# Performance work log

Measured on AMD Instinct MI355X. Metric: run time of the kernel, lower is better.

Reference implementation:

```python
import jax, jax.numpy as jnp
import numpy as np

N = 50000      # nodes
E = 800000     # edges (before self loops)
FE = 256       # expression features
FC = 128       # CNV features
H = 128        # hidden_channels
NC = 8         # num_classes
C = 512        # number of central nodes


def setup_inputs() -> dict:
    key = jax.random.key(0)
    ks = jax.random.split(key, 24)

    def lin(k, fi, fo):
        k1, k2 = jax.random.split(k)
        s = 1.0 / np.sqrt(fi)
        W = jax.random.uniform(k1, (fi, fo), jnp.float32, -s, s)
        b = jax.random.uniform(k2, (fo,), jnp.float32, -s, s)
        return W, b

    x = jax.random.normal(ks[0], (N, FE), jnp.float32)
    c = jax.random.normal(ks[1], (N, FC), jnp.float32)
    edge_index = jax.random.randint(ks[2], (2, E), 0, N, jnp.int32)
    central_idx = jax.random.randint(ks[3], (C,), 0, N, jnp.int32)

    W1e, b1e = lin(ks[4], FE, H)
    W2e, b2e = lin(ks[5], H, H)
    W1c, b1c = lin(ks[6], FC, H)
    W2c, b2c = lin(ks[7], H, H)
    Wm, bm = lin(ks[8], 2 * H, NC)
    Wp1, bp1 = lin(ks[9], NC, H)
    Wp2, bp2 = lin(ks[10], H, NC)

    return dict(
        x=x, c=c, edge_index=edge_index, central_idx=central_idx,
        me_x=jax.random.normal(ks[11], (FE,), jnp.float32),
        me_c=jax.random.normal(ks[12], (FC,), jnp.float32),
        W1e=W1e, b1e=b1e, eps1e=jnp.float32(0.0),
        W2e=W2e, b2e=b2e, eps2e=jnp.float32(0.0),
        W1c=W1c, b1c=b1c, eps1c=jnp.float32(0.0),
        W2c=W2c, b2c=b2c, eps2c=jnp.float32(0.0),
        Wm=Wm, bm=bm, Wp1=Wp1, bp1=bp1, Wp2=Wp2, bp2=bp2,
    )


def _gin_conv(h, src, dst, eps, W, b):
    # GINConv with nn = Linear: lin((1+eps)*x + sum_{j in N(i)} x_j)
    agg = jax.ops.segment_sum(h[src], dst, num_segments=N)  # scatter-add of messages
    return ((1.0 + eps) * h + agg) @ W + b


def reference(x, c, edge_index, central_idx, me_x, me_c,
              W1e, b1e, eps1e, W2e, b2e, eps2e,
              W1c, b1c, eps1c, W2c, b2c, eps2c,
              Wm, bm, Wp1, bp1, Wp2, bp2):
    lrelu = lambda v: jax.nn.leaky_relu(v, 0.2)

    # add self loops
    loops = jnp.arange(N, dtype=edge_index.dtype)
    src = jnp.concatenate([edge_index[0], loops])
    dst = jnp.concatenate([edge_index[1], loops])

    # replace exact-zero entries with learned missing embeddings (broadcast per row)
    x = jnp.where(x == 0, me_x[None, :], x)
    c = jnp.where(c == 0, me_c[None, :], c)

    x_exp = lrelu(_gin_conv(x, src, dst, eps1e, W1e, b1e))
    x_exp = lrelu(_gin_conv(x_exp, src, dst, eps2e, W2e, b2e))

    x_cnv = lrelu(_gin_conv(c, src, dst, eps1c, W1c, b1c))
    x_cnv = lrelu(_gin_conv(x_cnv, src, dst, eps2c, W2c, b2c))

    h = jnp.concatenate([x_exp, x_cnv], axis=1)          # [N, 2H]
    out = lrelu(h @ Wm + bm)                             # [N, NC]

    central = out[central_idx]                           # [C, NC]
    logits = jax.nn.relu(central @ Wp1 + bp1) @ Wp2 + bp2
    return out, logits
```

## Files before the change

### kernel.cpp

```cpp
#include <hip/hip_runtime.h>

typedef unsigned short u16;
typedef __attribute__((ext_vector_type(8))) short short8;
typedef __attribute__((ext_vector_type(4))) float floatx4;

__device__ __forceinline__ float b2f(unsigned int ubits) {
  union { unsigned int i; float f; } cv; cv.i = ubits << 16; return cv.f;
}
__device__ __forceinline__ float hi2f(unsigned int u) {
  union { unsigned int i; float f; } cv; cv.i = u & 0xffff0000u; return cv.f;
}
__device__ __forceinline__ float lo2f(unsigned int u) {
  union { unsigned int i; float f; } cv; cv.i = u << 16; return cv.f;
}
__device__ __forceinline__ u16 f2b(float f) {
  unsigned int u = __builtin_bit_cast(unsigned int, f);
  u += 0x7fffu + ((u >> 16) & 1u);
  return (u16)(u >> 16);
}
__device__ __forceinline__ float lrelu(float v) { return v > 0.f ? v : 0.2f * v; }
__device__ __forceinline__ float rdf(bool isbf, const void* p, int idx) {
  return isbf ? b2f((unsigned int)((const u16*)p)[idx]) : ((const float*)p)[idx];
}

__global__ __launch_bounds__(256) void init_kernel(int* __restrict__ deg, int n,
                                                   const u16* __restrict__ probe,
                                                   int* __restrict__ flag) {
  int i0 = (blockIdx.x * 256 + threadIdx.x) * 4;
  if (i0 + 3 < n) {
    *(int4*)(deg + i0) = make_int4(0, 0, 0, 0);
  } else {
    for (int j = 0; j < 4; j++) if (i0 + j < n) deg[i0 + j] = 0;
  }
  if (blockIdx.x == 0 && threadIdx.x < 64) {
    int lane = threadIdx.x;
    int cnt = 0;
    for (int i = lane; i < 256; i += 64) {
      unsigned int u = probe[i];
      unsigned int e = (u >> 7) & 0xFFu;
      if ((u & 0x7fffu) == 0 || (e >= 60 && e <= 191)) cnt++;
    }
#pragma unroll
    for (int off = 32; off; off >>= 1) cnt += __shfl_down(cnt, off, 64);
    if (lane == 0) *flag = (cnt >= 240) ? 1 : 0;
  }
}

__global__ __launch_bounds__(256) void hist_kernel(const int* __restrict__ dst, int E,
                                                   int* __restrict__ deg) {
  int i = blockIdx.x * 256 + threadIdx.x;
  if (i < E) atomicAdd(deg + dst[i], 1);
}

#define SCB 1024

__global__ __launch_bounds__(256) void scan_phaseA(const int* __restrict__ deg,
                                                   int* __restrict__ bsum, int n) {
  int i0 = blockIdx.x * SCB + threadIdx.x * 4;
  int s = 0;
  if (i0 + 3 < n) {
    int4 v = *(const int4*)(deg + i0);
    s = v.x + v.y + v.z + v.w;
  } else {
    for (int j = 0; j < 4; j++) if (i0 + j < n) s += deg[i0 + j];
  }
#pragma unroll
  for (int off = 32; off; off >>= 1) s += __shfl_down(s, off, 64);
  __shared__ int ws4[4];
  int lane = threadIdx.x & 63, wid = threadIdx.x >> 6;
  if (lane == 0) ws4[wid] = s;
  __syncthreads();
  if (threadIdx.x == 0) bsum[blockIdx.x] = ws4[0] + ws4[1] + ws4[2] + ws4[3];
}

__global__ void scan_phaseB(const int* __restrict__ bsum, int* __restrict__ boff,
                            int PB, int* __restrict__ rowptr, int n) {
  int lane = threadIdx.x;
  int v = (lane < PB) ? bsum[lane] : 0;
  int incl = v;
#pragma unroll
  for (int off = 1; off < 64; off <<= 1) {
    int t = __shfl_up(incl, off, 64);
    if (lane >= off) incl += t;
  }
  if (lane < PB) boff[lane] = incl - v;
  if (lane == 63) rowptr[n] = incl;
}

__global__ __launch_bounds__(256) void scan_phaseC(const int* __restrict__ deg,
                                                   const int* __restrict__ boff,
                                                   int* __restrict__ rowptr,
                                                   int* __restrict__ cursor, int n) {
  int i0 = blockIdx.x * SCB + threadIdx.x * 4;
  int v0 = 0, v1 = 0, v2 = 0, v3 = 0;
  if (i0 + 3 < n) {
    int4 v = *(const int4*)(deg + i0);
    v0 = v.x; v1 = v.y; v2 = v.z; v3 = v.w;
  } else {
    if (i0 < n) v0 = deg[i0];
    if (i0 + 1 < n) v1 = deg[i0 + 1];
    if (i0 + 2 < n) v2 = deg[i0 + 2];
    if (i0 + 3 < n) v3 = deg[i0 + 3];
  }
  int local = v0 + v1 + v2 + v3;
  int lane = threadIdx.x & 63, wid = threadIdx.x >> 6;
  int incl = local;
#pragma unroll
  for (int off = 1; off < 64; off <<= 1) {
    int t = __shfl_up(incl, off, 64);
    if (lane >= off) incl += t;
  }
  __shared__ int ws4[4];
  if (lane == 63) ws4[wid] = incl;
  __syncthreads();
  int woff = 0;
  for (int w = 0; w < wid; w++) woff += ws4[w];
  int run = boff[blockIdx.x] + woff + incl - local;
  if (i0 < n)     { rowptr[i0] = run;     cursor[i0] = run; }     run += v0;
  if (i0 + 1 < n) { rowptr[i0 + 1] = run; cursor[i0 + 1] = run; } run += v1;
  if (i0 + 2 < n) { rowptr[i0 + 2] = run; cursor[i0 + 2] = run; } run += v2;
  if (i0 + 3 < n) { rowptr[i0 + 3] = run; cursor[i0 + 3] = run; }
}

__global__ __launch_bounds__(256) void fill_kernel(const int* __restrict__ src,
                                                   const int* __restrict__ dst, int E,
                                                   int* __restrict__ cursor,
                                                   int* __restrict__ colarr) {
  int i = blockIdx.x * 256 + threadIdx.x;
  if (i < E) {
    int p = atomicAdd(cursor + dst[i], 1);
    colarr[p] = src[i];
  }
}

struct TWDesc {
  const void* W[5];
  int K[5];
  int Nc[5];
  int base[6];
};

__global__ __launch_bounds__(256) void transpose_all(TWDesc d, u16* __restrict__ out,
                                                     const int* __restrict__ flagp) {
  bool isbf = (*flagp != 0);
  int idx = blockIdx.x * 256 + threadIdx.x;
  if (idx >= d.base[5]) return;
  int s = 0;
  while (idx >= d.base[s + 1]) s++;
  int local = idx - d.base[s];
  int K = d.K[s], Nc = d.Nc[s];
  int nn = local / K;
  int k = local - nn * K;
  out[idx] = (nn < Nc) ? f2b(rdf(isbf, d.W[s], k * Nc + nn)) : (u16)0;
}

__device__ __forceinline__ short8 load_a_me(const void* Av, int lda, const void* me,
                                            int r, int k0, int q, bool isbf) {
  short8 a;
  if (isbf) {
    a = *(const short8*)((const u16*)Av + (long)r * lda + k0 + q * 8);
#pragma unroll
    for (int j = 0; j < 8; j++) {
      if (((u16)a[j] & 0x7fffu) == 0)
        a[j] = (short)((const u16*)me)[k0 + q * 8 + j];
    }
  } else {
    const float* A = (const float*)Av;
    const uint4* p = (const uint4*)(A + (long)r * lda + k0 + q * 8);
    uint4 w0 = p[0];
    uint4 w1 = p[1];
    unsigned int ww[8] = {w0.x, w0.y, w0.z, w0.w, w1.x, w1.y, w1.z, w1.w};
#pragma unroll
    for (int j = 0; j < 8; j++) {
      if ((ww[j] & 0x7fffffffu) == 0)
        a[j] = (short)f2b(((const float*)me)[k0 + q * 8 + j]);
      else
        a[j] = (short)f2b(__builtin_bit_cast(float, ww[j]));
    }
  }
  return a;
}

__global__ __launch_bounds__(256) void gemm_l1(
    const void* __restrict__ x, const void* __restrict__ cc,
    const void* __restrict__ mex, const void* __restrict__ mec,
    const u16* __restrict__ w1e_t, const u16* __restrict__ w1c_t,
    int M, u16* __restrict__ tb, const int* __restrict__ flagp) {
  bool isbf = (*flagp != 0);
  int wid = threadIdx.x >> 6;
  int lane = threadIdx.x & 63;
  int l15 = lane & 15;
  int q = lane >> 4;
  int row0 = blockIdx.x * 64 + wid * 16;
  int r = row0 + l15;
  if (r >= M) r = M - 1;

  floatx4 acce[8], accc[8];
#pragma unroll
  for (int n = 0; n < 8; n++) { acce[n] = (floatx4){0,0,0,0}; accc[n] = (floatx4){0,0,0,0}; }

  for (int k0 = 0; k0 < 256; k0 += 32) {
    short8 a = load_a_me(x, 256, mex, r, k0, q, isbf);
#pragma unroll
    for (int n = 0; n < 8; n++) {
      short8 b = *(const short8*)(w1e_t + (n * 16 + l15) * 256 + k0 + q * 8);
      acce[n] = __builtin_amdgcn_mfma_f32_16x16x32_bf16(a, b, acce[n], 0, 0, 0);
    }
  }
  for (int k0 = 0; k0 < 128; k0 += 32) {
    short8 a = load_a_me(cc, 128, mec, r, k0, q, isbf);
#pragma unroll
    for (int n = 0; n < 8; n++) {
      short8 b = *(const short8*)(w1c_t + (n * 16 + l15) * 128 + k0 + q * 8);
      accc[n] = __builtin_amdgcn_mfma_f32_16x16x32_bf16(a, b, accc[n], 0, 0, 0);
    }
  }
#pragma unroll
  for (int n = 0; n < 8; n++)
#pragma unroll
    for (int rr = 0; rr < 4; rr++) {
      int row = row0 + q * 4 + rr;
      if (row < M) {
        tb[(long)row * 256 + n * 16 + l15] = f2b(acce[n][rr]);
        tb[(long)row * 256 + 128 + n * 16 + l15] = f2b(accc[n][rr]);
      }
    }
}

__global__ __launch_bounds__(256) void gemm_l2(
    const u16* __restrict__ u,
    const u16* __restrict__ w2e_t, const u16* __restrict__ w2c_t,
    int M, u16* __restrict__ tb) {
  int wid = threadIdx.x >> 6;
  int lane = threadIdx.x & 63;
  int l15 = lane & 15;
  int q = lane >> 4;
  int row0 = blockIdx.x * 64 + wid * 16;
  int r = row0 + l15;
  if (r >= M) r = M - 1;

  floatx4 acce[8], accc[8];
#pragma unroll
  for (int n = 0; n < 8; n++) { acce[n] = (floatx4){0,0,0,0}; accc[n] = (floatx4){0,0,0,0}; }

  for (int k0 = 0; k0 < 128; k0 += 32) {
    short8 ae = *(const short8*)(u + (long)r * 256 + k0 + q * 8);
    short8 ac = *(const short8*)(u + (long)r * 256 + 128 + k0 + q * 8);
#pragma unroll
    for (int n = 0; n < 8; n++) {
      short8 be = *(const short8*)(w2e_t + (n * 16 + l15) * 128 + k0 + q * 8);
      short8 bc = *(const short8*)(w2c_t + (n * 16 + l15) * 128 + k0 + q * 8);
      acce[n] = __builtin_amdgcn_mfma_f32_16x16x32_bf16(ae, be, acce[n], 0, 0, 0);
      accc[n] = __builtin_amdgcn_mfma_f32_16x16x32_bf16(ac, bc, accc[n], 0, 0, 0);
    }
  }
#pragma unroll
  for (int n = 0; n < 8; n++)
#pragma unroll
    for (int rr = 0; rr < 4; rr++) {
      int row = row0 + q * 4 + rr;
      if (row < M) {
        tb[(long)row * 256 + n * 16 + l15] = f2b(acce[n][rr]);
        tb[(long)row * 256 + 128 + n * 16 + l15] = f2b(accc[n][rr]);
      }
    }
}

__global__ __launch_bounds__(256) void agg_kernel(
    const u16* __restrict__ t, const int* __restrict__ rowptr, const int* __restrict__ colarr,
    const void* __restrict__ epsE, const void* __restrict__ epsC,
    const void* __restrict__ bE, const void* __restrict__ bC,
    u16* __restrict__ u, int N, const int* __restrict__ flagp) {
  int node = blockIdx.x * 4 + (threadIdx.x >> 6);
  if (node >= N) return;
  bool isbf = (*flagp != 0);
  int lane = threadIdx.x & 63;
  int f0 = lane << 2;
  const u16* tb = t + f0;
  float a0 = 0.f, a1 = 0.f, a2 = 0.f, a3 = 0.f;
  int e = rowptr[node], e1 = rowptr[node + 1];
  for (; e + 4 <= e1; e += 4) {
    int c0 = colarr[e], c1 = colarr[e + 1], c2 = colarr[e + 2], c3 = colarr[e + 3];
    uint2 p0 = *(const uint2*)(tb + ((long)c0 << 8));
    uint2 p1 = *(const uint2*)(tb + ((long)c1 << 8));
    uint2 p2 = *(const uint2*)(tb + ((long)c2 << 8));
    uint2 p3 = *(const uint2*)(tb + ((long)c3 << 8));
    a0 += lo2f(p0.x); a1 += hi2f(p0.x); a2 += lo2f(p0.y); a3 += hi2f(p0.y);
    a0 += lo2f(p1.x); a1 += hi2f(p1.x); a2 += lo2f(p1.y); a3 += hi2f(p1.y);
    a0 += lo2f(p2.x); a1 += hi2f(p2.x); a2 += lo2f(p2.y); a3 += hi2f(p2.y);
    a0 += lo2f(p3.x); a1 += hi2f(p3.x); a2 += lo2f(p3.y); a3 += hi2f(p3.y);
  }
  for (; e < e1; e++) {
    int c = colarr[e];
    uint2 p = *(const uint2*)(tb + ((long)c << 8));
    a0 += lo2f(p.x); a1 += hi2f(p.x); a2 += lo2f(p.y); a3 += hi2f(p.y);
  }
  uint2 ps = *(const uint2*)(tb + ((long)node << 8));
  bool isE = (lane < 32);
  float eps2 = 2.0f + rdf(isbf, isE ? epsE : epsC, 0);
  const void* bp = isE ? bE : bC;
  int bi = isE ? f0 : (f0 - 128);
  a0 = lrelu(a0 + eps2 * lo2f(ps.x) + rdf(isbf, bp, bi + 0));
  a1 = lrelu(a1 + eps2 * hi2f(ps.x) + rdf(isbf, bp, bi + 1));
  a2 = lrelu(a2 + eps2 * lo2f(ps.y) + rdf(isbf, bp, bi + 2));
  a3 = lrelu(a3 + eps2 * hi2f(ps.y) + rdf(isbf, bp, bi + 3));
  uint2 o;
  o.x = ((unsigned int)f2b(a1) << 16) | f2b(a0);
  o.y = ((unsigned int)f2b(a3) << 16) | f2b(a2);
  *(uint2*)(u + ((long)node << 8) + f0) = o;
}

__global__ __launch_bounds__(256) void agg_head(
    const u16* __restrict__ t, const int* __restrict__ rowptr, const int* __restrict__ colarr,
    const void* __restrict__ epsE, const void* __restrict__ epsC,
    const void* __restrict__ bE, const void* __restrict__ bC,
    const u16* __restrict__ wm_t, const void* __restrict__ bm,
    float* __restrict__ out, int N, const int* __restrict__ flagp) {
  __shared__ float wmf[2048];
  __shared__ float bmf[8];
  bool isbf = (*flagp != 0);
  int tid = threadIdx.x;
  for (int i = tid; i < 2048; i += 256) wmf[i] = b2f((unsigned int)wm_t[i]);
  if (tid < 8) bmf[tid] = rdf(isbf, bm, tid);
  __syncthreads();

  int node = blockIdx.x * 4 + (tid >> 6);
  if (node >= N) return;
  int lane = tid & 63;
  int f0 = lane << 2;
  const u16* tb = t + f0;
  float a0 = 0.f, a1 = 0.f, a2 = 0.f, a3 = 0.f;
  int e = rowptr[node], e1 = rowptr[node + 1];
  for (; e + 4 <= e1; e += 4) {
    int c0 = colarr[e], c1 = colarr[e + 1], c2 = colarr[e + 2], c3 = colarr[e + 3];
    uint2 p0 = *(const uint2*)(tb + ((long)c0 << 8));
    uint2 p1 = *(const uint2*)(tb + ((long)c1 << 8));
    uint2 p2 = *(const uint2*)(tb + ((long)c2 << 8));
    uint2 p3 = *(const uint2*)(tb + ((long)c3 << 8));
    a0 += lo2f(p0.x); a1 += hi2f(p0.x); a2 += lo2f(p0.y); a3 += hi2f(p0.y);
    a0 += lo2f(p1.x); a1 += hi2f(p1.x); a2 += lo2f(p1.y); a3 += hi2f(p1.y);
    a0 += lo2f(p2.x); a1 += hi2f(p2.x); a2 += lo2f(p2.y); a3 += hi2f(p2.y);
    a0 += lo2f(p3.x); a1 += hi2f(p3.x); a2 += lo2f(p3.y); a3 += hi2f(p3.y);
  }
  for (; e < e1; e++) {
    int c = colarr[e];
    uint2 p = *(const uint2*)(tb + ((long)c << 8));
    a0 += lo2f(p.x); a1 += hi2f(p.x); a2 += lo2f(p.y); a3 += hi2f(p.y);
  }
  uint2 ps = *(const uint2*)(tb + ((long)node << 8));
  bool isE = (lane < 32);
  float eps2 = 2.0f + rdf(isbf, isE ? epsE : epsC, 0);
  const void* bp = isE ? bE : bC;
  int bi = isE ? f0 : (f0 - 128);
  a0 = lrelu(a0 + eps2 * lo2f(ps.x) + rdf(isbf, bp, bi + 0));
  a1 = lrelu(a1 + eps2 * hi2f(ps.x) + rdf(isbf, bp, bi + 1));
  a2 = lrelu(a2 + eps2 * lo2f(ps.y) + rdf(isbf, bp, bi + 2));
  a3 = lrelu(a3 + eps2 * hi2f(ps.y) + rdf(isbf, bp, bi + 3));

  float p[8];
#pragma unroll
  for (int col = 0; col < 8; col++) {
    float4 w = *(const float4*)&wmf[col * 256 + f0];
    p[col] = a0 * w.x + a1 * w.y + a2 * w.z + a3 * w.w;
  }
#pragma unroll
  for (int m = 1; m < 64; m <<= 1) {
#pragma unroll
    for (int col = 0; col < 8; col++) p[col] += __shfl_xor(p[col], m, 64);
  }
  if (lane == 0) {
    float4 o0, o1;
    o0.x = lrelu(p[0] + bmf[0]); o0.y = lrelu(p[1] + bmf[1]);
    o0.z = lrelu(p[2] + bmf[2]); o0.w = lrelu(p[3] + bmf[3]);
    o1.x = lrelu(p[4] + bmf[4]); o1.y = lrelu(p[5] + bmf[5]);
    o1.z = lrelu(p[6] + bmf[6]); o1.w = lrelu(p[7] + bmf[7]);
    *(float4*)(out + (long)node * 8) = o0;
    *(float4*)(out + (long)node * 8 + 4) = o1;
  }
}

__global__ __launch_bounds__(128) void mlp_kernel(
    const float* __restrict__ outbuf, const int* __restrict__ central,
    const void* __restrict__ Wp1, const void* __restrict__ bp1,
    const void* __restrict__ Wp2, const void* __restrict__ bp2,
    float* __restrict__ logits, const int* __restrict__ flagp) {
  __shared__ float h1[128];
  __shared__ float o[8];
  bool isbf = (*flagp != 0);
  int b = blockIdx.x, tid = threadIdx.x;
  int node = central[b];
  if (tid < 8) o[tid] = outbuf[node * 8 + tid];
  __syncthreads();
  float s = rdf(isbf, bp1, tid);
#pragma unroll
  for (int k = 0; k < 8; k++) s += o[k] * rdf(isbf, Wp1, k * 128 + tid);
  h1[tid] = fmaxf(s, 0.f);
  __syncthreads();
  if (tid < 8) {
    float s2 = rdf(isbf, bp2, tid);
    for (int k = 0; k < 128; k++) s2 += h1[k] * rdf(isbf, Wp2, k * 8 + tid);
    logits[b * 8 + tid] = s2;
  }
}

extern "C" void kernel_launch(void* const* d_in, const int* in_sizes, int n_in,
                              void* d_out, int out_size, void* d_ws, size_t ws_size,
                              hipStream_t stream) {
  const void* x    = d_in[0];
  const void* c    = d_in[1];
  const int* eidx  = (const int*)d_in[2];
  const int* cidx  = (const int*)d_in[3];
  const void* me_x = d_in[4];
  const void* me_c = d_in[5];
  const void* W1e  = d_in[6];
  const void* b1e  = d_in[7];
  const void* e1e  = d_in[8];
  const void* W2e  = d_in[9];
  const void* b2e  = d_in[10];
  const void* e2e  = d_in[11];
  const void* W1c  = d_in[12];
  const void* b1c  = d_in[13];
  const void* e1c  = d_in[14];
  const void* W2c  = d_in[15];
  const void* b2c  = d_in[16];
  const void* e2c  = d_in[17];
  const void* Wm   = d_in[18];
  const void* bm   = d_in[19];
  const void* Wp1  = d_in[20];
  const void* bp1  = d_in[21];
  const void* Wp2  = d_in[22];
  const void* bp2  = d_in[23];

  const int N = in_sizes[0] / 256;
  const int E = in_sizes[2] / 2;
  const int Cn = in_sizes[3];
  const int* src = eidx;
  const int* dst = eidx + E;

  char* ws = (char*)d_ws;
  int* deg    = (int*)(ws + 0);
  int* rowptr = (int*)(ws + 200192);
  int* cursor = (int*)(ws + 400384);
  int* colarr = (int*)(ws + 600576);
  u16* tbuf   = (u16*)(ws + 3800576);
  u16* ubuf   = (u16*)(ws + 29400576);
  u16* wt_all = (u16*)(ws + 55000576);
  int* flag   = (int*)(ws + 55172608);
  int* bsum   = (int*)(ws + 55172864);
  int* boff   = (int*)(ws + 55173120);

  u16* w1e_t = wt_all + 0;
  u16* w1c_t = wt_all + 32768;
  u16* w2e_t = wt_all + 49152;
  u16* w2c_t = wt_all + 65536;
  u16* wm_t  = wt_all + 81920;

  init_kernel<<<(N + 1023) / 1024, 256, 0, stream>>>(deg, N, (const u16*)x, flag);

  hist_kernel<<<(E + 255) / 256, 256, 0, stream>>>(dst, E, deg);
  int PB = (N + SCB - 1) / SCB;
  scan_phaseA<<<PB, 256, 0, stream>>>(deg, bsum, N);
  scan_phaseB<<<1, 64, 0, stream>>>(bsum, boff, PB, rowptr, N);
  scan_phaseC<<<PB, 256, 0, stream>>>(deg, boff, rowptr, cursor, N);
  fill_kernel<<<(E + 255) / 256, 256, 0, stream>>>(src, dst, E, cursor, colarr);

  TWDesc td;
  td.W[0] = W1e; td.K[0] = 256; td.Nc[0] = 128;
  td.W[1] = W1c; td.K[1] = 128; td.Nc[1] = 128;
  td.W[2] = W2e; td.K[2] = 128; td.Nc[2] = 128;
  td.W[3] = W2c; td.K[3] = 128; td.Nc[3] = 128;
  td.W[4] = Wm;  td.K[4] = 256; td.Nc[4] = 8;
  td.base[0] = 0; td.base[1] = 32768; td.base[2] = 49152;
  td.base[3] = 65536; td.base[4] = 81920; td.base[5] = 86016;
  transpose_all<<<(86016 + 255) / 256, 256, 0, stream>>>(td, wt_all, flag);

  int gb = (N + 63) / 64;
  gemm_l1<<<gb, 256, 0, stream>>>(x, c, me_x, me_c, w1e_t, w1c_t, N, tbuf, flag);
  agg_kernel<<<(N + 3) / 4, 256, 0, stream>>>(tbuf, rowptr, colarr,
      e1e, e1c, b1e, b1c, ubuf, N, flag);
  gemm_l2<<<gb, 256, 0, stream>>>(ubuf, w2e_t, w2c_t, N, tbuf);
  agg_head<<<(N + 3) / 4, 256, 0, stream>>>(tbuf, rowptr, colarr,
      e2e, e2c, b2e, b2c, wm_t, bm, (float*)d_out, N, flag);
  mlp_kernel<<<Cn, 128, 0, stream>>>((const float*)d_out, cidx,
      Wp1, bp1, Wp2, bp2, (float*)d_out + (size_t)N * 8, flag);
}
```

Baseline: 464.5 us.

## Split neighbor gather across half-waves with 16-byte loads and index prefetch

```diff
diff --git a/kernel.cpp b/kernel.cpp
--- a/kernel.cpp
+++ b/kernel.cpp
@@ -3,6 +3,7 @@
 typedef unsigned short u16;
 typedef __attribute__((ext_vector_type(8))) short short8;
 typedef __attribute__((ext_vector_type(4))) float floatx4;
+typedef __attribute__((ext_vector_type(2))) float floatx2;
 
 __device__ __forceinline__ float b2f(unsigned int ubits) {
   union { unsigned int i; float f; } cv; cv.i = ubits << 16; return cv.f;
@@ -21,6 +22,9 @@
 __device__ __forceinline__ float lrelu(float v) { return v > 0.f ? v : 0.2f * v; }
 __device__ __forceinline__ float rdf(bool isbf, const void* p, int idx) {
   return isbf ? b2f((unsigned int)((const u16*)p)[idx]) : ((const float*)p)[idx];
+}
+__device__ __forceinline__ floatx2 up2(unsigned int u) {
+  return (floatx2){lo2f(u), hi2f(u)};
 }
 
 __global__ __launch_bounds__(256) void init_kernel(int* __restrict__ deg, int n,
@@ -266,48 +270,88 @@
     }
 }
 
+__device__ __forceinline__ void gin_gather(
+    const u16* __restrict__ t, const int* __restrict__ rowptr,
+    const int* __restrict__ colarr, const u16* __restrict__ zrow,
+    int node, int E, int eh, long fb, floatx2 aa[4]) {
+  const char* base = (const char*)t;
+  const char* zb = (const char*)zrow + fb;
+#pragma unroll
+  for (int j = 0; j < 4; j++) aa[j] = (floatx2){0.f, 0.f};
+  int e = rowptr[node], e1 = rowptr[node + 1];
+  int ee0 = e + eh, ee1 = e + 2 + eh;
+  int c0 = colarr[ee0 < E ? ee0 : E - 1];
+  int c1 = colarr[ee1 < E ? ee1 : E - 1];
+  for (; e + 4 <= e1; e += 4) {
+    int ne0 = e + 4 + eh, ne1 = e + 6 + eh;
+    int nc0 = colarr[ne0 < E ? ne0 : E - 1];
+    int nc1 = colarr[ne1 < E ? ne1 : E - 1];
+    uint4 w0 = *(const uint4*)(base + ((long)c0 << 9) + fb);
+    uint4 w1 = *(const uint4*)(base + ((long)c1 << 9) + fb);
+    aa[0] += up2(w0.x); aa[1] += up2(w0.y); aa[2] += up2(w0.z); aa[3] += up2(w0.w);
+    aa[0] += up2(w1.x); aa[1] += up2(w1.y); aa[2] += up2(w1.z); aa[3] += up2(w1.w);
+    c0 = nc0; c1 = nc1;
+  }
+  if (e < e1) {
+    const char* p0 = (e + eh < e1)     ? base + ((long)c0 << 9) + fb : zb;
+    const char* p1 = (e + 2 + eh < e1) ? base + ((long)c1 << 9) + fb : zb;
+    uint4 w0 = *(const uint4*)p0;
+    uint4 w1 = *(const uint4*)p1;
+    aa[0] += up2(w0.x); aa[1] += up2(w0.y); aa[2] += up2(w0.z); aa[3] += up2(w0.w);
+    aa[0] += up2(w1.x); aa[1] += up2(w1.y); aa[2] += up2(w1.z); aa[3] += up2(w1.w);
+  }
+#pragma unroll
+  for (int j = 0; j < 4; j++) {
+    aa[j].x += __shfl_xor(aa[j].x, 32, 64);
+    aa[j].y += __shfl_xor(aa[j].y, 32, 64);
+  }
+}
+
+__device__ __forceinline__ void gin_eps_bias(
+    bool isbf, int fl, const u16* __restrict__ t, int node, long fb,
+    const void* epsE, const void* epsC, const void* bE, const void* bC,
+    floatx2 aa[4]) {
+  uint4 s = *(const uint4*)((const char*)t + ((long)node << 9) + fb);
+  bool isE = (fl < 16);
+  float eps2 = 2.0f + rdf(isbf, isE ? epsE : epsC, 0);
+  const void* bp = isE ? bE : bC;
+  int bi = (fl << 3) - (isE ? 0 : 128);
+  aa[0].x = lrelu(aa[0].x + eps2 * lo2f(s.x) + rdf(isbf, bp, bi + 0));
+  aa[0].y = lrelu(aa[0].y + eps2 * hi2f(s.x) + rdf(isbf, bp, bi + 1));
+  aa[1].x = lrelu(aa[1].x + eps2 * lo2f(s.y) + rdf(isbf, bp, bi + 2));
+  aa[1].y = lrelu(aa[1].y + eps2 * hi2f(s.y) + rdf(isbf, bp, bi + 3));
+  aa[2].x = lrelu(aa[2].x + eps2 * lo2f(s.z) + rdf(isbf, bp, bi + 4));
+  aa[2].y = lrelu(aa[2].y + eps2 * hi2f(s.z) + rdf(isbf, bp, bi + 5));
+  aa[3].x = lrelu(aa[3].x + eps2 * lo2f(s.w) + rdf(isbf, bp, bi + 6));
+  aa[3].y = lrelu(aa[3].y + eps2 * hi2f(s.w) + rdf(isbf, bp, bi + 7));
+}
+
 __global__ __launch_bounds__(256) void agg_kernel(
     const u16* __restrict__ t, const int* __restrict__ rowptr, const int* __restrict__ colarr,
     const void* __restrict__ epsE, const void* __restrict__ epsC,
     const void* __restrict__ bE, const void* __restrict__ bC,
-    u16* __restrict__ u, int N, const int* __restrict__ flagp) {
+    u16* __restrict__ u, int N, int E, const u16* __restrict__ zrow,
+    const int* __restrict__ flagp) {
   int node = blockIdx.x * 4 + (threadIdx.x >> 6);
   if (node >= N) return;
   bool isbf = (*flagp != 0);
   int lane = threadIdx.x & 63;
-  int f0 = lane << 2;
-  const u16* tb = t + f0;
-  float a0 = 0.f, a1 = 0.f, a2 = 0.f, a3 = 0.f;
-  int e = rowptr[node], e1 = rowptr[node + 1];
-  for (; e + 4 <= e1; e += 4) {
-    int c0 = colarr[e], c1 = colarr[e + 1], c2 = colarr[e + 2], c3 = colarr[e + 3];
-    uint2 p0 = *(const uint2*)(tb + ((long)c0 << 8));
-    uint2 p1 = *(const uint2*)(tb + ((long)c1 << 8));
-    uint2 p2 = *(const uint2*)(tb + ((long)c2 << 8));
-    uint2 p3 = *(const uint2*)(tb + ((long)c3 << 8));
-    a0 += lo2f(p0.x); a1 += hi2f(p0.x); a2 += lo2f(p0.y); a3 += hi2f(p0.y);
-    a0 += lo2f(p1.x); a1 += hi2f(p1.x); a2 += lo2f(p1.y); a3 += hi2f(p1.y);
-    a0 += lo2f(p2.x); a1 += hi2f(p2.x); a2 += lo2f(p2.y); a3 += hi2f(p2.y);
-    a0 += lo2f(p3.x); a1 += hi2f(p3.x); a2 += lo2f(p3.y); a3 += hi2f(p3.y);
-  }
-  for (; e < e1; e++) {
-    int c = colarr[e];
-    uint2 p = *(const uint2*)(tb + ((long)c << 8));
-    a0 += lo2f(p.x); a1 += hi2f(p.x); a2 += lo2f(p.y); a3 += hi2f(p.y);
-  }
-  uint2 ps = *(const uint2*)(tb + ((long)node << 8));
-  bool isE = (lane < 32);
-  float eps2 = 2.0f + rdf(isbf, isE ? epsE : epsC, 0);
-  const void* bp = isE ? bE : bC;
-  int bi = isE ? f0 : (f0 - 128);
-  a0 = lrelu(a0 + eps2 * lo2f(ps.x) + rdf(isbf, bp, bi + 0));
-  a1 = lrelu(a1 + eps2 * hi2f(ps.x) + rdf(isbf, bp, bi + 1));
-  a2 = lrelu(a2 + eps2 * lo2f(ps.y) + rdf(isbf, bp, bi + 2));
-  a3 = lrelu(a3 + eps2 * hi2f(ps.y) + rdf(isbf, bp, bi + 3));
-  uint2 o;
-  o.x = ((unsigned int)f2b(a1) << 16) | f2b(a0);
-  o.y = ((unsigned int)f2b(a3) << 16) | f2b(a2);
-  *(uint2*)(u + ((long)node << 8) + f0) = o;
+  int eh = lane >> 5;
+  int fl = lane & 31;
+  long fb = (long)fl << 4;
+
+  floatx2 aa[4];
+  gin_gather(t, rowptr, colarr, zrow, node, E, eh, fb, aa);
+  gin_eps_bias(isbf, fl, t, node, fb, epsE, epsC, bE, bC, aa);
+
+  if (eh == 0) {
+    uint4 o;
+    o.x = ((unsigned int)f2b(aa[0].y) << 16) | f2b(aa[0].x);
+    o.y = ((unsigned int)f2b(aa[1].y) << 16) | f2b(aa[1].x);
+    o.z = ((unsigned int)f2b(aa[2].y) << 16) | f2b(aa[2].x);
+    o.w = ((unsigned int)f2b(aa[3].y) << 16) | f2b(aa[3].x);
+    *(uint4*)(u + ((long)node << 8) + (fl << 3)) = o;
+  }
 }
 
 __global__ __launch_bounds__(256) void agg_head(
@@ -315,7 +359,8 @@
     const void* __restrict__ epsE, const void* __restrict__ epsC,
     const void* __restrict__ bE, const void* __restrict__ bC,
     const u16* __restrict__ wm_t, const void* __restrict__ bm,
-    float* __restrict__ out, int N, const int* __restrict__ flagp) {
+    float* __restrict__ out, int N, int E, const u16* __restrict__ zrow,
+    const int* __restrict__ flagp) {
   __shared__ float wmf[2048];
   __shared__ float bmf[8];
   bool isbf = (*flagp != 0);
@@ -327,44 +372,25 @@
   int node = blockIdx.x * 4 + (tid >> 6);
   if (node >= N) return;
   int lane = tid & 63;
-  int f0 = lane << 2;
-  const u16* tb = t + f0;
-  float a0 = 0.f, a1 = 0.f, a2 = 0.f, a3 = 0.f;
-  int e = rowptr[node], e1 = rowptr[node + 1];
-  for (; e + 4 <= e1; e += 4) {
-    int c0 = colarr[e], c1 = colarr[e + 1], c2 = colarr[e + 2], c3 = colarr[e + 3];
-    uint2 p0 = *(const uint2*)(tb + ((long)c0 << 8));
-    uint2 p1 = *(const uint2*)(tb + ((long)c1 << 8));
-    uint2 p2 = *(const uint2*)(tb + ((long)c2 << 8));
-    uint2 p3 = *(const uint2*)(tb + ((long)c3 << 8));
-    a0 += lo2f(p0.x); a1 += hi2f(p0.x); a2 += lo2f(p0.y); a3 += hi2f(p0.y);
-    a0 += lo2f(p1.x); a1 += hi2f(p1.x); a2 += lo2f(p1.y); a3 += hi2f(p1.y);
-    a0 += lo2f(p2.x); a1 += hi2f(p2.x); a2 += lo2f(p2.y); a3 += hi2f(p2.y);
-    a0 += lo2f(p3.x); a1 += hi2f(p3.x); a2 += lo2f(p3.y); a3 += hi2f(p3.y);
-  }
-  for (; e < e1; e++) {
-    int c = colarr[e];
-    uint2 p = *(const uint2*)(tb + ((long)c << 8));
-    a0 += lo2f(p.x); a1 += hi2f(p.x); a2 += lo2f(p.y); a3 += hi2f(p.y);
-  }
-  uint2 ps = *(const uint2*)(tb + ((long)node << 8));
-  bool isE = (lane < 32);
-  float eps2 = 2.0f + rdf(isbf, isE ? epsE : epsC, 0);
-  const void* bp = isE ? bE : bC;
-  int bi = isE ? f0 : (f0 - 128);
-  a0 = lrelu(a0 + eps2 * lo2f(ps.x) + rdf(isbf, bp, bi + 0));
-  a1 = lrelu(a1 + eps2 * hi2f(ps.x) + rdf(isbf, bp, bi + 1));
-  a2 = lrelu(a2 + eps2 * lo2f(ps.y) + rdf(isbf, bp, bi + 2));
-  a3 = lrelu(a3 + eps2 * hi2f(ps.y) + rdf(isbf, bp, bi + 3));
-
+  int eh = lane >> 5;
+  int fl = lane & 31;
+  long fb = (long)fl << 4;
+
+  floatx2 aa[4];
+  gin_gather(t, rowptr, colarr, zrow, node, E, eh, fb, aa);
+  gin_eps_bias(isbf, fl, t, node, fb, epsE, epsC, bE, bC, aa);
+
+  int f0 = fl << 3;
   float p[8];
 #pragma unroll
   for (int col = 0; col < 8; col++) {
-    float4 w = *(const float4*)&wmf[col * 256 + f0];
-    p[col] = a0 * w.x + a1 * w.y + a2 * w.z + a3 * w.w;
-  }
-#pragma unroll
-  for (int m = 1; m < 64; m <<= 1) {
+    float4 wA = *(const float4*)&wmf[col * 256 + f0];
+    float4 wB = *(const float4*)&wmf[col * 256 + f0 + 4];
+    p[col] = aa[0].x * wA.x + aa[0].y * wA.y + aa[1].x * wA.z + aa[1].y * wA.w
+           + aa[2].x * wB.x + aa[2].y * wB.y + aa[3].x * wB.z + aa[3].y * wB.w;
+  }
+#pragma unroll
+  for (int m = 1; m < 32; m <<= 1) {
 #pragma unroll
     for (int col = 0; col < 8; col++) p[col] += __shfl_xor(p[col], m, 64);
   }
@@ -454,6 +480,7 @@
   u16* w2e_t = wt_all + 49152;
   u16* w2c_t = wt_all + 65536;
   u16* wm_t  = wt_all + 81920;
+  const u16* zrow = wt_all + 83968;
 
   init_kernel<<<(N + 1023) / 1024, 256, 0, stream>>>(deg, N, (const u16*)x, flag);
 
@@ -477,10 +504,10 @@
   int gb = (N + 63) / 64;
   gemm_l1<<<gb, 256, 0, stream>>>(x, c, me_x, me_c, w1e_t, w1c_t, N, tbuf, flag);
   agg_kernel<<<(N + 3) / 4, 256, 0, stream>>>(tbuf, rowptr, colarr,
-      e1e, e1c, b1e, b1c, ubuf, N, flag);
+      e1e, e1c, b1e, b1c, ubuf, N, E, zrow, flag);
   gemm_l2<<<gb, 256, 0, stream>>>(ubuf, w2e_t, w2c_t, N, tbuf);
   agg_head<<<(N + 3) / 4, 256, 0, stream>>>(tbuf, rowptr, colarr,
-      e2e, e2c, b2e, b2c, wm_t, bm, (float*)d_out, N, flag);
+      e2e, e2c, b2e, b2c, wm_t, bm, (float*)d_out, N, E, zrow, flag);
   mlp_kernel<<<Cn, 128, 0, stream>>>((const float*)d_out, cidx,
       Wp1, bp1, Wp2, bp2, (float*)d_out + (size_t)N * 8, flag);
 }
```

New measurement: 496.4 us. 1.07x slower.
